# Performance work log

Hardware: AMD Instinct MI355X
Metric: run time of the kernel (lower is better)

## Reference

```python
import jax, jax.numpy as jnp
import numpy as np

BETA = 0.25

def _encoder(x, W0, b0, W1, b1, W2, b2):
    # MLP: Linear+ReLU, Linear+ReLU, Linear (dims 768->512->256->64)
    h = jax.nn.relu(x @ W0 + b0)
    h = jax.nn.relu(h @ W1 + b1)
    return h @ W2 + b2

def _rvq(z, codebooks):
    # Residual vector quantization over L=4 levels (structurally distinct loop).
    residual = z
    x_q = jnp.zeros_like(z)
    losses = []
    codes = []
    for l in range(codebooks.shape[0]):
        cb = codebooks[l]  # [K, e]
        # squared L2 distances [N, K] via expansion (avoids materializing [N,K,e])
        d = (jnp.sum(residual * residual, axis=1, keepdims=True)
             - 2.0 * residual @ cb.T
             + jnp.sum(cb * cb, axis=1))
        idx = jnp.argmin(d, axis=1)           # [N]
        q = cb[idx]                            # gather [N, e]
        # codebook loss + beta * commitment loss
        loss = (jnp.mean((jax.lax.stop_gradient(q) - residual) ** 2)
                + BETA * jnp.mean((q - jax.lax.stop_gradient(residual)) ** 2))
        losses.append(loss)
        # straight-through estimator
        q_st = residual + jax.lax.stop_gradient(q - residual)
        residual = residual - q_st
        x_q = x_q + q_st
        codes.append(idx)
    rq_loss = jnp.mean(jnp.stack(losses))
    return x_q, rq_loss, jnp.stack(codes)  # codes: [L, N] int


def setup_inputs() -> dict:
    key = jax.random.key(0)
    ks = jax.random.split(key, 8)
    N, D = 131072, 768
    dims = [768, 512, 256, 64]
    x = jax.random.normal(ks[0], (N, D), dtype=jnp.float32)
    W0 = jax.random.normal(ks[1], (dims[0], dims[1]), dtype=jnp.float32) * (1.0 / np.sqrt(dims[0]))
    b0 = jnp.zeros((dims[1],), dtype=jnp.float32)
    W1 = jax.random.normal(ks[2], (dims[1], dims[2]), dtype=jnp.float32) * (1.0 / np.sqrt(dims[1]))
    b1 = jnp.zeros((dims[2],), dtype=jnp.float32)
    W2 = jax.random.normal(ks[3], (dims[2], dims[3]), dtype=jnp.float32) * (1.0 / np.sqrt(dims[2]))
    b2 = jnp.zeros((dims[3],), dtype=jnp.float32)
    codebooks = jax.random.normal(ks[4], (4, 256, 64), dtype=jnp.float32)
    return {"x": x, "W0": W0, "b0": b0, "W1": W1, "b1": b1, "W2": W2, "b2": b2,
            "codebooks": codebooks}


def reference(x, W0, b0, W1, b1, W2, b2, codebooks):
    z = _encoder(x, W0, b0, W1, b1, W2, b2)          # [N, 64]
    x_q, rq_loss, codes = _rvq(z, codebooks)
    return x_q, rq_loss, codes
```

## Files before the change

### kernel.cpp

```cpp
#include <hip/hip_runtime.h>
#include <hip/hip_bf16.h>


typedef double d2v __attribute__((ext_vector_type(2)));

template<bool RELU, int NCOLSHIFT>
__global__ __launch_bounds__(256) void gemm128(
    const float* __restrict__ A, const float* __restrict__ W,
    const float* __restrict__ bias, float* __restrict__ C,
    int M, int N, int K)
{
    __shared__ float As[16][132];
    __shared__ float Bs[16][132];

    const int nwg  = gridDim.x * gridDim.y;
    const int id   = blockIdx.y * gridDim.x + blockIdx.x;
    const int xcd  = id & 7;
    const int rest = id >> 3;
    const int q8   = nwg >> 3, r8 = nwg & 7;
    const int wg   = (xcd < r8 ? xcd * (q8 + 1) : r8 * (q8 + 1) + (xcd - r8) * q8) + rest;
    const int NCOL = 1 << NCOLSHIFT;

    const int col0 = (wg & (NCOL - 1)) * 128;
    const int row0 = (wg >> NCOLSHIFT) * 128;

    const int tid = threadIdx.x;
    const int tx = tid & 15;
    const int ty = tid >> 4;

    const float* Ab = A + (size_t)row0 * K;
    const float* Wb = W + col0;

    const int am0 = tid >> 2,          ak0 = (tid & 3) * 4;
    const int am1 = (tid + 256) >> 2,  ak1 = ((tid + 256) & 3) * 4;
    const int bk0 = tid >> 5,          bn0 = (tid & 31) * 4;
    const int bk1 = (tid + 256) >> 5,  bn1 = ((tid + 256) & 31) * 4;

    float acc[8][8] = {};

    float4 sa0 = *reinterpret_cast<const float4*>(Ab + (size_t)am0 * K + ak0);
    float4 sa1 = *reinterpret_cast<const float4*>(Ab + (size_t)am1 * K + ak1);
    float4 sb0 = *reinterpret_cast<const float4*>(Wb + (size_t)bk0 * N + bn0);
    float4 sb1 = *reinterpret_cast<const float4*>(Wb + (size_t)bk1 * N + bn1);
    As[ak0 + 0][am0] = sa0.x; As[ak0 + 1][am0] = sa0.y;
    As[ak0 + 2][am0] = sa0.z; As[ak0 + 3][am0] = sa0.w;
    As[ak1 + 0][am1] = sa1.x; As[ak1 + 1][am1] = sa1.y;
    As[ak1 + 2][am1] = sa1.z; As[ak1 + 3][am1] = sa1.w;
    *reinterpret_cast<float4*>(&Bs[bk0][bn0]) = sb0;
    *reinterpret_cast<float4*>(&Bs[bk1][bn1]) = sb1;
    __syncthreads();

    for (int k0 = 0; k0 < K; k0 += 16) {
        const bool hasNext = (k0 + 16 < K);
        if (hasNext) {
            const float* An = Ab + k0 + 16;
            const float* Wn = Wb + (size_t)(k0 + 16) * N;
            sa0 = *reinterpret_cast<const float4*>(An + (size_t)am0 * K + ak0);
            sa1 = *reinterpret_cast<const float4*>(An + (size_t)am1 * K + ak1);
            sb0 = *reinterpret_cast<const float4*>(Wn + (size_t)bk0 * N + bn0);
            sb1 = *reinterpret_cast<const float4*>(Wn + (size_t)bk1 * N + bn1);
        }

#pragma unroll
        for (int kk = 0; kk < 16; ++kk) {
            float4 a0 = *reinterpret_cast<const float4*>(&As[kk][ty * 4]);
            float4 a1 = *reinterpret_cast<const float4*>(&As[kk][64 + ty * 4]);
            float4 b0 = *reinterpret_cast<const float4*>(&Bs[kk][tx * 4]);
            float4 b1 = *reinterpret_cast<const float4*>(&Bs[kk][64 + tx * 4]);
            float ar[8] = {a0.x, a0.y, a0.z, a0.w, a1.x, a1.y, a1.z, a1.w};
            float br[8] = {b0.x, b0.y, b0.z, b0.w, b1.x, b1.y, b1.z, b1.w};
#pragma unroll
            for (int m = 0; m < 8; ++m)
#pragma unroll
                for (int n = 0; n < 8; ++n)
                    acc[m][n] = fmaf(ar[m], br[n], acc[m][n]);
        }

        if (hasNext) {
            __syncthreads();
            As[ak0 + 0][am0] = sa0.x; As[ak0 + 1][am0] = sa0.y;
            As[ak0 + 2][am0] = sa0.z; As[ak0 + 3][am0] = sa0.w;
            As[ak1 + 0][am1] = sa1.x; As[ak1 + 1][am1] = sa1.y;
            As[ak1 + 2][am1] = sa1.z; As[ak1 + 3][am1] = sa1.w;
            *reinterpret_cast<float4*>(&Bs[bk0][bn0]) = sb0;
            *reinterpret_cast<float4*>(&Bs[bk1][bn1]) = sb1;
            __syncthreads();
        }
    }

    float bl[4], bh[4];
#pragma unroll
    for (int n = 0; n < 4; ++n) {
        bl[n] = bias[col0 + tx * 4 + n];
        bh[n] = bias[col0 + 64 + tx * 4 + n];
    }
#pragma unroll
    for (int half = 0; half < 2; ++half) {
#pragma unroll
        for (int r = 0; r < 4; ++r) {
            int m = half * 4 + r;
            int row = row0 + half * 64 + ty * 4 + r;
            float4 lo, hi;
            lo.x = acc[m][0] + bl[0]; lo.y = acc[m][1] + bl[1];
            lo.z = acc[m][2] + bl[2]; lo.w = acc[m][3] + bl[3];
            hi.x = acc[m][4] + bh[0]; hi.y = acc[m][5] + bh[1];
            hi.z = acc[m][6] + bh[2]; hi.w = acc[m][7] + bh[3];
            if (RELU) {
                lo.x = fmaxf(lo.x, 0.f); lo.y = fmaxf(lo.y, 0.f);
                lo.z = fmaxf(lo.z, 0.f); lo.w = fmaxf(lo.w, 0.f);
                hi.x = fmaxf(hi.x, 0.f); hi.y = fmaxf(hi.y, 0.f);
                hi.z = fmaxf(hi.z, 0.f); hi.w = fmaxf(hi.w, 0.f);
            }
            float* Cr = C + (size_t)row * N + col0;
            *reinterpret_cast<float4*>(Cr + tx * 4) = lo;
            *reinterpret_cast<float4*>(Cr + 64 + tx * 4) = hi;
        }
    }
}

template<bool RELU>
__global__ __launch_bounds__(256) void gemm_bias(
    const float* __restrict__ A, const float* __restrict__ W,
    const float* __restrict__ bias, float* __restrict__ C,
    int M, int N, int K)
{
    __shared__ float As[16][132];
    __shared__ float Bs[16][68];

    const int tid = threadIdx.x;
    const int tx = tid & 15;
    const int ty = tid >> 4;
    const int col0 = blockIdx.x * 64;
    const int row0 = blockIdx.y * 128;

    const float* Ab = A + (size_t)row0 * K;
    const float* Wb = W + col0;

    float acc[8][4] = {};

    for (int k0 = 0; k0 < K; k0 += 16) {
#pragma unroll
        for (int i = 0; i < 2; ++i) {
            int pos = tid + i * 256;
            int m  = pos >> 2;
            int k4 = (pos & 3) * 4;
            float4 v = *reinterpret_cast<const float4*>(Ab + (size_t)m * K + k0 + k4);
            As[k4 + 0][m] = v.x; As[k4 + 1][m] = v.y;
            As[k4 + 2][m] = v.z; As[k4 + 3][m] = v.w;
        }
        {
            int kk = tid >> 4;
            int n4 = (tid & 15) * 4;
            float4 v = *reinterpret_cast<const float4*>(Wb + (size_t)(k0 + kk) * N + n4);
            *reinterpret_cast<float4*>(&Bs[kk][n4]) = v;
        }
        __syncthreads();
#pragma unroll
        for (int kk = 0; kk < 16; ++kk) {
            float4 a0 = *reinterpret_cast<const float4*>(&As[kk][ty * 8]);
            float4 a1 = *reinterpret_cast<const float4*>(&As[kk][ty * 8 + 4]);
            float4 bv = *reinterpret_cast<const float4*>(&Bs[kk][tx * 4]);
            float a[8] = {a0.x, a0.y, a0.z, a0.w, a1.x, a1.y, a1.z, a1.w};
            float b[4] = {bv.x, bv.y, bv.z, bv.w};
#pragma unroll
            for (int m = 0; m < 8; ++m)
#pragma unroll
                for (int n = 0; n < 4; ++n)
                    acc[m][n] = fmaf(a[m], b[n], acc[m][n]);
        }
        __syncthreads();
    }

    float bv[4];
#pragma unroll
    for (int n = 0; n < 4; ++n) bv[n] = bias[col0 + tx * 4 + n];
#pragma unroll
    for (int m = 0; m < 8; ++m) {
        int row = row0 + ty * 8 + m;
        float4 o;
        float v0 = acc[m][0] + bv[0];
        float v1 = acc[m][1] + bv[1];
        float v2 = acc[m][2] + bv[2];
        float v3 = acc[m][3] + bv[3];
        if (RELU) {
            v0 = fmaxf(v0, 0.f); v1 = fmaxf(v1, 0.f);
            v2 = fmaxf(v2, 0.f); v3 = fmaxf(v3, 0.f);
        }
        o.x = v0; o.y = v1; o.z = v2; o.w = v3;
        *reinterpret_cast<float4*>(C + (size_t)row * N + col0 + tx * 4) = o;
    }
}

__global__ void cb_norms(const float* __restrict__ cb,
                         double* __restrict__ cn64, float* __restrict__ cnf) {
    int c = blockIdx.x * 64 + threadIdx.x;
    const float* p = cb + (size_t)c * 64;
    double s = 0.0;
#pragma unroll
    for (int j = 0; j < 64; ++j) {
        double v = (double)p[j];
        s = fma(v, v, s);
    }
    cn64[c] = s;
    cnf[c]  = (float)s;
}

__global__ void build_cbw(const float* __restrict__ cb, double* __restrict__ cbw) {
    int i = blockIdx.x * 256 + threadIdx.x;
    cbw[i] = -2.0 * (double)cb[i];
}

#define EGUARD 1e-3

__device__ __forceinline__ double rank64(const double* __restrict__ p,
                                         double R0, const float (&rd)[64]) {
    double c0 = 0.0, c1 = 0.0, c2 = 0.0, c3 = 0.0;
#pragma unroll
    for (int j = 0; j < 16; ++j) {
        d2v x = *reinterpret_cast<const d2v*>(p + j * 4);
        d2v y = *reinterpret_cast<const d2v*>(p + j * 4 + 2);
        c0 = fma(x[0], (double)rd[j * 4 + 0], c0);
        c1 = fma(x[1], (double)rd[j * 4 + 1], c1);
        c2 = fma(y[0], (double)rd[j * 4 + 2], c2);
        c3 = fma(y[1], (double)rd[j * 4 + 3], c3);
    }
    return R0 + ((c0 + c1) + (c2 + c3));
}

__global__ __launch_bounds__(256) void rvq_v5(
    const float* __restrict__ z,
    const float* __restrict__ cbf,
    const double* __restrict__ cbw,
    const double* __restrict__ cn64,
    const float* __restrict__ cnf,
    float* __restrict__ xq,
    float* __restrict__ codes,
    double* __restrict__ partials,
    int row0, int Ntot)
{
    __shared__ float sd1[4][64];
    __shared__ float sd2[4][64];
    __shared__ int   si1[4][64];
    __shared__ int   si2[4][64];

    const int tid  = threadIdx.x;
    const int lane = tid & 63;
    const int w    = tid >> 6;
    const int wu   = __builtin_amdgcn_readfirstlane(w);
    const int blk  = blockIdx.x;
    const int grow0 = row0 + blk * 64;

    float rd[64];
    const float* zr = z + (size_t)(blk * 64 + lane) * 64;
#pragma unroll
    for (int q = 0; q < 16; ++q) {
        float4 v = *reinterpret_cast<const float4*>(zr + q * 4);
        rd[q * 4 + 0] = v.x; rd[q * 4 + 1] = v.y;
        rd[q * 4 + 2] = v.z; rd[q * 4 + 3] = v.w;
    }

    double sse = 0.0;

    for (int lv = 0; lv < 4; ++lv) {
        const int cbase = lv * 256;
        __syncthreads();

        const float* cwl = cbf + (size_t)(cbase + wu * 64) * 64;
        const float* cnl = cnf + cbase + wu * 64;

        float d1 = 3.4e38f, d2 = 3.4e38f;
        int   i1 = 0,       i2 = 0;

#pragma unroll 2
        for (int c = 0; c < 64; ++c) {
            const float* cp = cwl + c * 64;
            float acc8[8];
#pragma unroll
            for (int q = 0; q < 8; ++q) {
                float4 va = *reinterpret_cast<const float4*>(cp + q * 8);
                float4 vb = *reinterpret_cast<const float4*>(cp + q * 8 + 4);
                float t = 0.f;
                t = fmaf(va.x, rd[q * 8 + 0], t);
                t = fmaf(va.y, rd[q * 8 + 1], t);
                t = fmaf(va.z, rd[q * 8 + 2], t);
                t = fmaf(va.w, rd[q * 8 + 3], t);
                t = fmaf(vb.x, rd[q * 8 + 4], t);
                t = fmaf(vb.y, rd[q * 8 + 5], t);
                t = fmaf(vb.z, rd[q * 8 + 6], t);
                t = fmaf(vb.w, rd[q * 8 + 7], t);
                acc8[q] = t;
            }
            float dot = ((acc8[0] + acc8[1]) + (acc8[2] + acc8[3]))
                      + ((acc8[4] + acc8[5]) + (acc8[6] + acc8[7]));
            float d = fmaf(-2.f, dot, cnl[c]);
            int code = wu * 64 + c;
            if (d < d1) { d2 = d1; i2 = i1; d1 = d; i1 = code; }
            else if (d < d2) { d2 = d; i2 = code; }
        }

        sd1[w][lane] = d1; si1[w][lane] = i1;
        sd2[w][lane] = d2; si2[w][lane] = i2;
        __syncthreads();

        float bd1 = sd1[0][lane]; int bi1 = si1[0][lane]; int wstar = 0;
#pragma unroll
        for (int ww = 1; ww < 4; ++ww) {
            float dd = sd1[ww][lane]; int ii = si1[ww][lane];
            if (dd < bd1 || (dd == bd1 && ii < bi1)) { bd1 = dd; bi1 = ii; wstar = ww; }
        }
        float d2g = 3.4e38f; int i2g = 0;
#pragma unroll
        for (int ww = 0; ww < 4; ++ww) {
            float dd = (ww == wstar) ? sd2[ww][lane] : sd1[ww][lane];
            int   ii = (ww == wstar) ? si2[ww][lane] : si1[ww][lane];
            if (dd < d2g) { d2g = dd; i2g = ii; }
        }

        double R1 = rank64(cbw + (size_t)(cbase + bi1) * 64, cn64[cbase + bi1], rd);
        double R2 = rank64(cbw + (size_t)(cbase + i2g) * 64, cn64[cbase + i2g], rd);
        int ci; double Rw;
        if (R1 < R2 || (R1 == R2 && bi1 < i2g)) { ci = bi1; Rw = R1; }
        else                                    { ci = i2g; Rw = R2; }

        if (!(Rw < (double)d2g - EGUARD)) {
            float l8f = fminf(fminf(sd2[0][lane], sd2[1][lane]),
                              fminf(sd2[2][lane], sd2[3][lane]));
            double L8 = (double)l8f;
            double Rm = 1.0e300; int im = 0;
#pragma unroll
            for (int ww = 0; ww < 4; ++ww) {
#pragma unroll
                for (int k = 0; k < 2; ++k) {
                    int cc = k ? si2[ww][lane] : si1[ww][lane];
                    double R = rank64(cbw + (size_t)(cbase + cc) * 64,
                                      cn64[cbase + cc], rd);
                    if (R < Rm || (R == Rm && cc < im)) { Rm = R; im = cc; }
                }
            }
            if (Rm < L8 - EGUARD) {
                ci = im;
            } else {
                double dmin = 1.0e300; int imin = 0;
#pragma unroll 1
                for (int c = 0; c < 256; ++c) {
                    double R = rank64(cbw + (size_t)(cbase + c) * 64,
                                      cn64[cbase + c], rd);
                    if (R < dmin) { dmin = R; imin = c; }
                }
                ci = imin;
            }
        }

        const float* qp = cbf + (size_t)(cbase + ci) * 64;
        double lsse = 0.0;
#pragma unroll
        for (int q = 0; q < 16; ++q) {
            float4 qv = *reinterpret_cast<const float4*>(qp + q * 4);
            float r0 = rd[q * 4 + 0], r1 = rd[q * 4 + 1];
            float r2 = rd[q * 4 + 2], r3 = rd[q * 4 + 3];
            if (w == 0) {
                float e0 = qv.x - r0, e1 = qv.y - r1;
                float e2 = qv.z - r2, e3 = qv.w - r3;
                lsse = fma((double)e0, (double)e0, lsse);
                lsse = fma((double)e1, (double)e1, lsse);
                lsse = fma((double)e2, (double)e2, lsse);
                lsse = fma((double)e3, (double)e3, lsse);
            }
            rd[q * 4 + 0] = r0 - qv.x; rd[q * 4 + 1] = r1 - qv.y;
            rd[q * 4 + 2] = r2 - qv.z; rd[q * 4 + 3] = r3 - qv.w;
        }
        if (w == 0) {
            sse += lsse;
            codes[(size_t)lv * Ntot + grow0 + lane] = (float)ci;
        }
    }

    if (w == 0) {
        size_t base = (size_t)(grow0 + lane) * 64;
#pragma unroll
        for (int q = 0; q < 16; ++q) {
            float4 zv = *reinterpret_cast<const float4*>(zr + q * 4);
            float4 o;
            o.x = zv.x - rd[q * 4 + 0];
            o.y = zv.y - rd[q * 4 + 1];
            o.z = zv.z - rd[q * 4 + 2];
            o.w = zv.w - rd[q * 4 + 3];
            *reinterpret_cast<float4*>(xq + base + q * 4) = o;
        }
        double s = sse;
#pragma unroll
        for (int off = 32; off > 0; off >>= 1) {
            union { double d; int i[2]; } u; u.d = s;
            u.i[0] = __shfl_down(u.i[0], off, 64);
            u.i[1] = __shfl_down(u.i[1], off, 64);
            s += u.d;
        }
        if (lane == 0) partials[grow0 >> 6] = s;
    }
}

__global__ void loss_final(const double* __restrict__ partials, int n,
                           float* __restrict__ out, double scale) {
    __shared__ double s[256];
    double acc = 0.0;
    for (int i = threadIdx.x; i < n; i += 256) acc += partials[i];
    s[threadIdx.x] = acc;
    __syncthreads();
    for (int off = 128; off > 0; off >>= 1) {
        if ((int)threadIdx.x < off) s[threadIdx.x] += s[threadIdx.x + off];
        __syncthreads();
    }
    if (threadIdx.x == 0) *out = (float)(s[0] * scale);
}

extern "C" void kernel_launch(void* const* d_in, const int* in_sizes, int n_in,
                              void* d_out, int out_size, void* d_ws, size_t ws_size,
                              hipStream_t stream) {
    const float* x  = (const float*)d_in[0];
    const float* W0 = (const float*)d_in[1];
    const float* b0 = (const float*)d_in[2];
    const float* W1 = (const float*)d_in[3];
    const float* b1 = (const float*)d_in[4];
    const float* W2 = (const float*)d_in[5];
    const float* b2 = (const float*)d_in[6];
    const float* cb = (const float*)d_in[7];

    const int N = in_sizes[0] / 768;

    float* out   = (float*)d_out;
    float* xq    = out;
    float* loss  = out + (size_t)N * 64;
    float* codes = loss + 1;

    const int nblk_total = N / 64;
    const size_t tail_floats = 131072 + 2048 + 2 * (size_t)nblk_total + 1024 + 64;

    size_t avail = ws_size / 4;
    avail = (avail > tail_floats) ? (avail - tail_floats) : 0;
    int Nc = (int)(avail / 832);
    Nc = (Nc / 128) * 128;
    if (Nc > N) Nc = N;
    if (Nc < 128) Nc = 128;

    float* ws = (float*)d_ws;
    float* h0 = ws;
    float* h1 = h0 + (size_t)Nc * 512;
    float* z  = h1 + (size_t)Nc * 256;
    double* cbw      = (double*)(ws + (size_t)Nc * 832);
    double* cn64     = cbw + 65536;
    double* partials = cn64 + 1024;
    float*  cnf      = (float*)(partials + nblk_total);

    cb_norms <<<16, 64, 0, stream>>>(cb, cn64, cnf);
    build_cbw<<<256, 256, 0, stream>>>(cb, cbw);

    for (int r0 = 0; r0 < N; r0 += Nc) {
        int cur = (N - r0 < Nc) ? (N - r0) : Nc;
        gemm128<true, 2><<<dim3(512 / 128, cur / 128), 256, 0, stream>>>(
            x + (size_t)r0 * 768, W0, b0, h0, cur, 512, 768);
        gemm128<true, 1><<<dim3(256 / 128, cur / 128), 256, 0, stream>>>(
            h0, W1, b1, h1, cur, 256, 512);
        gemm_bias<false><<<dim3(1, cur / 128), 256, 0, stream>>>(
            h1, W2, b2, z, cur, 64, 256);
        rvq_v5<<<cur / 64, 256, 0, stream>>>(
            z, cb, cbw, cn64, cnf, xq, codes, partials, r0, N);
    }

    loss_final<<<1, 256, 0, stream>>>(partials, nblk_total, loss,
                                      1.25 / (4.0 * (double)N * 64.0));
}
```

Before: 2.907 ms.

## Use a single wavefront per RVQ block scanning all codes

The RVQ kernel drops its four-wave split of the 256 codewords in favor of one 64-lane wavefront per 64-row block, where each lane scans all 256 codes serially. This removes the shared-memory top-2 merge, the per-level barriers and the duplicated residual updates across waves. In exchange each block does four times more serial work per lane and there are four times fewer waves in flight per row. The fallback path also shrinks from an 8-candidate recheck to a direct full rescan.

```diff
diff --git a/kernel.cpp b/kernel.cpp
--- a/kernel.cpp
+++ b/kernel.cpp
@@ -227,7 +227,7 @@
     return R0 + ((c0 + c1) + (c2 + c3));
 }
 
-__global__ __launch_bounds__(256) void rvq_v5(
+__global__ __launch_bounds__(64) void rvq_w1(
     const float* __restrict__ z,
     const float* __restrict__ cbf,
     const double* __restrict__ cbw,
@@ -238,15 +238,7 @@
     double* __restrict__ partials,
     int row0, int Ntot)
 {
-    __shared__ float sd1[4][64];
-    __shared__ float sd2[4][64];
-    __shared__ int   si1[4][64];
-    __shared__ int   si2[4][64];
-
-    const int tid  = threadIdx.x;
-    const int lane = tid & 63;
-    const int w    = tid >> 6;
-    const int wu   = __builtin_amdgcn_readfirstlane(w);
+    const int lane = threadIdx.x;
     const int blk  = blockIdx.x;
     const int grow0 = row0 + blk * 64;
 
@@ -263,16 +255,14 @@
 
     for (int lv = 0; lv < 4; ++lv) {
         const int cbase = lv * 256;
-        __syncthreads();
-
-        const float* cwl = cbf + (size_t)(cbase + wu * 64) * 64;
-        const float* cnl = cnf + cbase + wu * 64;
+        const float* cwl = cbf + (size_t)cbase * 64;
+        const float* cnl = cnf + cbase;
 
         float d1 = 3.4e38f, d2 = 3.4e38f;
         int   i1 = 0,       i2 = 0;
 
 #pragma unroll 2
-        for (int c = 0; c < 64; ++c) {
+        for (int c = 0; c < 256; ++c) {
             const float* cp = cwl + c * 64;
             float acc8[8];
 #pragma unroll
@@ -293,62 +283,26 @@
             float dot = ((acc8[0] + acc8[1]) + (acc8[2] + acc8[3]))
                       + ((acc8[4] + acc8[5]) + (acc8[6] + acc8[7]));
             float d = fmaf(-2.f, dot, cnl[c]);
-            int code = wu * 64 + c;
-            if (d < d1) { d2 = d1; i2 = i1; d1 = d; i1 = code; }
-            else if (d < d2) { d2 = d; i2 = code; }
-        }
-
-        sd1[w][lane] = d1; si1[w][lane] = i1;
-        sd2[w][lane] = d2; si2[w][lane] = i2;
-        __syncthreads();
-
-        float bd1 = sd1[0][lane]; int bi1 = si1[0][lane]; int wstar = 0;
-#pragma unroll
-        for (int ww = 1; ww < 4; ++ww) {
-            float dd = sd1[ww][lane]; int ii = si1[ww][lane];
-            if (dd < bd1 || (dd == bd1 && ii < bi1)) { bd1 = dd; bi1 = ii; wstar = ww; }
-        }
-        float d2g = 3.4e38f; int i2g = 0;
-#pragma unroll
-        for (int ww = 0; ww < 4; ++ww) {
-            float dd = (ww == wstar) ? sd2[ww][lane] : sd1[ww][lane];
-            int   ii = (ww == wstar) ? si2[ww][lane] : si1[ww][lane];
-            if (dd < d2g) { d2g = dd; i2g = ii; }
-        }
-
-        double R1 = rank64(cbw + (size_t)(cbase + bi1) * 64, cn64[cbase + bi1], rd);
-        double R2 = rank64(cbw + (size_t)(cbase + i2g) * 64, cn64[cbase + i2g], rd);
+            if (d < d1) { d2 = d1; i2 = i1; d1 = d; i1 = c; }
+            else if (d < d2) { d2 = d; i2 = c; }
+        }
+
+        double R1 = rank64(cbw + (size_t)(cbase + i1) * 64, cn64[cbase + i1], rd);
+        double R2 = rank64(cbw + (size_t)(cbase + i2) * 64, cn64[cbase + i2], rd);
         int ci; double Rw;
-        if (R1 < R2 || (R1 == R2 && bi1 < i2g)) { ci = bi1; Rw = R1; }
-        else                                    { ci = i2g; Rw = R2; }
-
-        if (!(Rw < (double)d2g - EGUARD)) {
-            float l8f = fminf(fminf(sd2[0][lane], sd2[1][lane]),
-                              fminf(sd2[2][lane], sd2[3][lane]));
-            double L8 = (double)l8f;
-            double Rm = 1.0e300; int im = 0;
-#pragma unroll
-            for (int ww = 0; ww < 4; ++ww) {
-#pragma unroll
-                for (int k = 0; k < 2; ++k) {
-                    int cc = k ? si2[ww][lane] : si1[ww][lane];
-                    double R = rank64(cbw + (size_t)(cbase + cc) * 64,
-                                      cn64[cbase + cc], rd);
-                    if (R < Rm || (R == Rm && cc < im)) { Rm = R; im = cc; }
-                }
+        if (R1 < R2)      { ci = i1; Rw = R1; }
+        else if (R2 < R1) { ci = i2; Rw = R2; }
+        else              { ci = (i1 < i2) ? i1 : i2; Rw = R1; }
+
+        if (!(Rw < (double)d2 - EGUARD)) {
+            double dmin = 1.0e300; int imin = 0;
+#pragma unroll 1
+            for (int c = 0; c < 256; ++c) {
+                double R = rank64(cbw + (size_t)(cbase + c) * 64,
+                                  cn64[cbase + c], rd);
+                if (R < dmin) { dmin = R; imin = c; }
             }
-            if (Rm < L8 - EGUARD) {
-                ci = im;
-            } else {
-                double dmin = 1.0e300; int imin = 0;
-#pragma unroll 1
-                for (int c = 0; c < 256; ++c) {
-                    double R = rank64(cbw + (size_t)(cbase + c) * 64,
-                                      cn64[cbase + c], rd);
-                    if (R < dmin) { dmin = R; imin = c; }
-                }
-                ci = imin;
-            }
+            ci = imin;
         }
 
         const float* qp = cbf + (size_t)(cbase + ci) * 64;
@@ -358,24 +312,20 @@
             float4 qv = *reinterpret_cast<const float4*>(qp + q * 4);
             float r0 = rd[q * 4 + 0], r1 = rd[q * 4 + 1];
             float r2 = rd[q * 4 + 2], r3 = rd[q * 4 + 3];
-            if (w == 0) {
-                float e0 = qv.x - r0, e1 = qv.y - r1;
-                float e2 = qv.z - r2, e3 = qv.w - r3;
-                lsse = fma((double)e0, (double)e0, lsse);
-                lsse = fma((double)e1, (double)e1, lsse);
-                lsse = fma((double)e2, (double)e2, lsse);
-                lsse = fma((double)e3, (double)e3, lsse);
-            }
+            float e0 = qv.x - r0, e1 = qv.y - r1;
+            float e2 = qv.z - r2, e3 = qv.w - r3;
+            lsse = fma((double)e0, (double)e0, lsse);
+            lsse = fma((double)e1, (double)e1, lsse);
+            lsse = fma((double)e2, (double)e2, lsse);
+            lsse = fma((double)e3, (double)e3, lsse);
             rd[q * 4 + 0] = r0 - qv.x; rd[q * 4 + 1] = r1 - qv.y;
             rd[q * 4 + 2] = r2 - qv.z; rd[q * 4 + 3] = r3 - qv.w;
         }
-        if (w == 0) {
-            sse += lsse;
-            codes[(size_t)lv * Ntot + grow0 + lane] = (float)ci;
-        }
-    }
-
-    if (w == 0) {
+        sse += lsse;
+        codes[(size_t)lv * Ntot + grow0 + lane] = (float)ci;
+    }
+
+    {
         size_t base = (size_t)(grow0 + lane) * 64;
 #pragma unroll
         for (int q = 0; q < 16; ++q) {
@@ -462,7 +412,7 @@
             h0, W1, b1, h1, cur, 256, 512);
         gemm_bias<false><<<dim3(1, cur / 128), 256, 0, stream>>>(
             h1, W2, b2, z, cur, 64, 256);
-        rvq_v5<<<cur / 64, 256, 0, stream>>>(
+        rvq_w1<<<cur / 64, 64, 0, stream>>>(
             z, cb, cbw, cn64, cnf, xq, codes, partials, r0, N);
     }
 
```

Result: faster. 2.498 ms (median of 2 runs) (-14.1%).
